# Performance work log

Hardware: AMD Instinct MI355X
Metric: run time of the kernel (lower is better)

The kernel has to match this reference:

```python
import jax, jax.numpy as jnp
import numpy as np
from functools import partial

D_MODEL = 768
N_LAYER = 2
VOCAB = 50264  # 50257 padded to multiple of 8
D_STATE = 16
D_INNER = 2 * D_MODEL
DT_RANK = 48
D_CONV = 4
EPS = 1e-5
ZOH_EPS = 1e-7
B, L = 2, 1024


def setup_inputs() -> dict:
    key = jax.random.key(0)
    ks = jax.random.split(key, 16)
    s = 0.02
    inp = {
        'input_ids': jax.random.randint(ks[0], (B, L), 0, VOCAB, dtype=jnp.int32),
        'embedding': jax.random.normal(ks[1], (VOCAB, D_MODEL), jnp.float32) * s,
        'in_w': jax.random.normal(ks[2], (N_LAYER, D_MODEL, 2 * D_INNER), jnp.float32) * s,
        'in_b': jnp.zeros((N_LAYER, 2 * D_INNER), jnp.float32),
        'conv_w': jax.random.normal(ks[3], (N_LAYER, D_INNER, D_CONV), jnp.float32) * s,
        'conv_b': jnp.zeros((N_LAYER, D_INNER), jnp.float32),
        'xproj_w': jax.random.normal(ks[4], (N_LAYER, D_INNER, DT_RANK + 2 * D_STATE), jnp.float32) * s,
        'dt_w': jax.random.normal(ks[5], (N_LAYER, DT_RANK, D_INNER), jnp.float32) * s,
        'dt_b': jnp.zeros((N_LAYER, D_INNER), jnp.float32),
        'A_log': jnp.broadcast_to(jnp.log(jnp.arange(1, D_STATE + 1, dtype=jnp.float32))[None, None, :], (N_LAYER, D_INNER, D_STATE)).copy(),
        'Dp': jnp.ones((N_LAYER, D_INNER), jnp.float32),
        'out_w': jax.random.normal(ks[6], (N_LAYER, D_INNER, D_MODEL), jnp.float32) * s,
        'out_b': jnp.zeros((N_LAYER, D_MODEL), jnp.float32),
        'norm_w': jnp.ones((N_LAYER, D_MODEL), jnp.float32),
        'normf_w': jnp.ones((D_MODEL,), jnp.float32),
    }
    return inp


def rmsnorm(x, w):
    return x * jax.lax.rsqrt(jnp.mean(x * x, axis=-1, keepdims=True) + EPS) * w


def mamba_block(x, in_w, in_b, conv_w, conv_b, xproj_w, dt_w, dt_b, A_log, Dp, out_w, out_b):
    # x: (b, l, d_model)
    xr = x @ in_w + in_b                       # (b, l, 2*d_inner)
    xi, res = jnp.split(xr, 2, axis=-1)        # each (b, l, d_inner)
    # causal depthwise conv1d (torch pads d_conv-1 both sides then truncates to l)
    xc = jnp.transpose(xi, (0, 2, 1))          # (b, d_inner, l)
    xc = jax.lax.conv_general_dilated(
        xc, conv_w[:, None, :], (1,), [(D_CONV - 1, 0)],
        dimension_numbers=('NCH', 'OIH', 'NCH'), feature_group_count=D_INNER)
    xc = xc + conv_b[None, :, None]
    u = jax.nn.silu(jnp.transpose(xc, (0, 2, 1)))  # (b, l, d_inner)
    res = jax.nn.silu(res)
    # generate time-varying SSM params
    dbc = u @ xproj_w                          # (b, l, dt_rank + 2n)
    dt, Bm, Cm = jnp.split(dbc, [DT_RANK, DT_RANK + D_STATE], axis=-1)
    delta = jax.nn.softplus(dt @ dt_w + dt_b)  # (b, l, d_inner)
    A = -jnp.exp(A_log)                        # (d_inner, n)
    # ZOH discretization
    dA = jnp.exp(jnp.einsum('bld,dn->bldn', delta, A))            # (b,l,d_in,n)
    zoh = (dA - 1.0) / (A + ZOH_EPS)                               # (b,l,d_in,n)
    dBu = zoh * Bm[:, :, None, :] * u[..., None]                   # (b,l,d_in,n)
    # selective scan over l
    def step(s, inputs):
        dA_t, dBu_t, C_t = inputs              # (b,d_in,n),(b,d_in,n),(b,n)
        s = dA_t * s + dBu_t
        y = jnp.einsum('bdn,bn->bd', s, C_t)
        return s, y
    s0 = jnp.zeros((u.shape[0], D_INNER, D_STATE), u.dtype)
    _, ys = jax.lax.scan(step, s0, (jnp.moveaxis(dA, 1, 0), jnp.moveaxis(dBu, 1, 0), jnp.moveaxis(Cm, 1, 0)))
    y = jnp.moveaxis(ys, 0, 1) + u * Dp        # (b, l, d_inner)
    y = y * res
    return y @ out_w + out_b


def forward(input_ids, embedding, in_w, in_b, conv_w, conv_b, xproj_w, dt_w, dt_b, A_log, Dp, out_w, out_b, norm_w, normf_w):
    x = embedding[input_ids]                   # (b, l, d_model)
    for i in range(N_LAYER):
        mixed = mamba_block(x, in_w[i], in_b[i], conv_w[i], conv_b[i], xproj_w[i],
                            dt_w[i], dt_b[i], A_log[i], Dp[i], out_w[i], out_b[i])
        x = rmsnorm(mixed + x, norm_w[i])      # ResidualBlock: norm(mixer(x)+x)
    x = rmsnorm(x, normf_w)
    return x @ embedding.T                     # tied lm_head, (b, l, vocab)


def reference(input_ids, embedding, in_w, in_b, conv_w, conv_b, xproj_w, dt_w, dt_b, A_log, Dp, out_w, out_b, norm_w, normf_w):
    return forward(input_ids, embedding, in_w, in_b, conv_w, conv_b, xproj_w,
                   dt_w, dt_b, A_log, Dp, out_w, out_b, norm_w, normf_w)
```

## Files before the change

kernel.cpp:

```cpp
#include <hip/hip_runtime.h>
#include <math.h>
#include <stdint.h>

#define BB 2
#define LL 1024
#define DM 768
#define NL 2
#define VV 50264
#define VPAD 50304
#define DS 16
#define DI 1536
#define DR 48
#define DC 4
#define MM (BB*LL)

#define CH 32
#define NC (LL/CH)

#define KS 8

#define TS 64
#define KT 16

typedef __attribute__((ext_vector_type(8))) short short8;
typedef __attribute__((ext_vector_type(4))) float f32x4;

#define AS3(p) ((__attribute__((address_space(3))) unsigned int*)(unsigned int)(uintptr_t)(p))
#define AS1(p) ((const __attribute__((address_space(1))) unsigned int*)(uintptr_t)(p))

__device__ __forceinline__ unsigned short f2bf(float v) {
    union { float f; unsigned u; } x; x.f = v;
    unsigned r = x.u + 0x7fffu + ((x.u >> 16) & 1u);
    return (unsigned short)(r >> 16);
}

__global__ __launch_bounds__(256) void embed_kernel(
    const int* __restrict__ ids, const float* __restrict__ emb,
    float* __restrict__ x, unsigned short* __restrict__ x16)
{
    int m = blockIdx.x;
    int v = ids[m];
    const float* src = emb + (size_t)v * DM;
    float* dst = x + (size_t)m * DM;
    unsigned short* dst16 = x16 + (size_t)m * DM;
    for (int i = threadIdx.x; i < DM; i += 256) {
        float f = src[i];
        dst[i] = f;
        dst16[i] = f2bf(f);
    }
}

__global__ __launch_bounds__(256) void emb_convert_kernel(
    const float* __restrict__ emb, unsigned short* __restrict__ out)
{
    size_t i8 = (size_t)blockIdx.x * 256 + threadIdx.x;
    size_t row = i8 / 96;
    size_t col8 = (i8 - row * 96) * 8;
    if (row >= VPAD) return;
    ushort4 o0, o1;
    if (row < VV) {
        const float* p = emb + row * DM + col8;
        float4 v0 = *(const float4*)p;
        float4 v1 = *(const float4*)(p + 4);
        o0.x = f2bf(v0.x); o0.y = f2bf(v0.y); o0.z = f2bf(v0.z); o0.w = f2bf(v0.w);
        o1.x = f2bf(v1.x); o1.y = f2bf(v1.y); o1.z = f2bf(v1.z); o1.w = f2bf(v1.w);
    } else {
        o0 = make_ushort4(0, 0, 0, 0);
        o1 = o0;
    }
    unsigned short* op = out + row * DM + col8;
    *(ushort4*)op = o0;
    *(ushort4*)(op + 4) = o1;
}

__global__ __launch_bounds__(256) void transpose_bf16_kernel(
    const float* __restrict__ in, unsigned short* __restrict__ out, int R, int C)
{
    __shared__ float t[32][33];
    int l = blockIdx.z;
    int r0 = blockIdx.y * 32, c0 = blockIdx.x * 32;
    int tx = threadIdx.x & 31, ty = threadIdx.x >> 5;
    const float* ip = in + (size_t)l * R * C;
    unsigned short* op = out + (size_t)l * C * R;
    #pragma unroll
    for (int j = 0; j < 32; j += 8)
        t[ty + j][tx] = ip[(size_t)(r0 + ty + j) * C + c0 + tx];
    __syncthreads();
    #pragma unroll
    for (int j = 0; j < 32; j += 8)
        op[(size_t)(c0 + ty + j) * R + r0 + tx] = f2bf(t[tx][ty + j]);
}

__global__ __launch_bounds__(256) void gemm_mfma_bt(
    const unsigned short* __restrict__ A, const unsigned short* __restrict__ B,
    const float* __restrict__ bias, const float* __restrict__ resid,
    float* __restrict__ C, int M, int N, int K, int MT, int NTILES)
{
    int T = MT * NTILES;
    int q = T >> 3, r = T & 7;
    int orig = blockIdx.x;
    int xcd = orig & 7, u = orig >> 3;
    int wg = (xcd < r ? xcd * (q + 1) : r * (q + 1) + (xcd - r) * q) + u;
    int mt = wg % MT, nt = wg / MT;

    __shared__ unsigned short As[3][128 * 32];
    __shared__ unsigned short Bs[3][128 * 32];
    int tid = threadIdx.x;
    int w = tid >> 6, lane = tid & 63;
    int m0 = mt * 128, n0 = nt * 128;

    int rA = lane >> 2;
    int kb = (lane & 3) * 8;
    const unsigned short* gA0 = A + (size_t)(m0 + w * 16 + rA) * K + kb;
    const unsigned short* gA1 = gA0 + (size_t)64 * K;
    const unsigned short* gB0 = B + (size_t)(n0 + w * 16 + rA) * K + kb;
    const unsigned short* gB1 = gB0 + (size_t)64 * K;

    int lr = lane & 15, lk = lane >> 4;
    int wr = (w >> 1) * 64, wc = (w & 1) * 64;

    f32x4 acc[4][4] = {};

#define STAGE(k0, buf) do { \
    __builtin_amdgcn_global_load_lds(AS1(gA0 + (k0)), AS3(&As[buf][(w * 16) * 32]), 16, 0, 0); \
    __builtin_amdgcn_global_load_lds(AS1(gA1 + (k0)), AS3(&As[buf][(64 + w * 16) * 32]), 16, 0, 0); \
    __builtin_amdgcn_global_load_lds(AS1(gB0 + (k0)), AS3(&Bs[buf][(w * 16) * 32]), 16, 0, 0); \
    __builtin_amdgcn_global_load_lds(AS1(gB1 + (k0)), AS3(&Bs[buf][(64 + w * 16) * 32]), 16, 0, 0); \
} while (0)

#define COMPUTE(buf) do { \
    short8 a[4], b[4]; \
    _Pragma("unroll") \
    for (int f = 0; f < 4; ++f) \
        a[f] = *(const short8*)&As[buf][(wr + f * 16 + lr) * 32 + lk * 8]; \
    _Pragma("unroll") \
    for (int f = 0; f < 4; ++f) \
        b[f] = *(const short8*)&Bs[buf][(wc + f * 16 + lr) * 32 + lk * 8]; \
    _Pragma("unroll") \
    for (int i = 0; i < 4; ++i) \
        _Pragma("unroll") \
        for (int j = 0; j < 4; ++j) \
            acc[i][j] = __builtin_amdgcn_mfma_f32_16x16x32_bf16(a[i], b[j], acc[i][j], 0, 0, 0); \
} while (0)

    int nsteps = K / 32;
    STAGE(0, 0);
    STAGE(32, 1);
    asm volatile("s_waitcnt vmcnt(4)" ::: "memory");
    __builtin_amdgcn_s_barrier();
    __builtin_amdgcn_sched_barrier(0);

    for (int t = 0; t < nsteps; ++t) {
        int cur = t % 3;
        if (t + 2 < nsteps)
            STAGE((t + 2) * 32, (t + 2) % 3);
        COMPUTE(cur);
        if (t + 1 < nsteps) {
            if (t + 2 < nsteps)
                asm volatile("s_waitcnt vmcnt(4)" ::: "memory");
            else
                asm volatile("s_waitcnt vmcnt(0)" ::: "memory");
            __builtin_amdgcn_s_barrier();
            __builtin_amdgcn_sched_barrier(0);
        }
    }

#undef STAGE
#undef COMPUTE

    #pragma unroll
    for (int i = 0; i < 4; ++i) {
        int row = m0 + wr + i * 16 + lk * 4;
        #pragma unroll
        for (int j = 0; j < 4; ++j) {
            int col = n0 + wc + j * 16 + lr;
            if (col < N) {
                float bv = bias ? bias[col] : 0.f;
                #pragma unroll
                for (int r2 = 0; r2 < 4; ++r2) {
                    float v = acc[i][j][r2] + bv;
                    if (resid) v += resid[(size_t)(row + r2) * N + col];
                    C[(size_t)(row + r2) * N + col] = v;
                }
            }
        }
    }
}

__global__ __launch_bounds__(512) void gemm_logits(
    const unsigned short* __restrict__ A, const unsigned short* __restrict__ B,
    float* __restrict__ C, int M, int N, int K, int MT, int NTILES)
{
    int T = MT * NTILES;
    int q = T >> 3, r = T & 7;
    int orig = blockIdx.x;
    int xcd = orig & 7, u = orig >> 3;
    int wg = (xcd < r ? xcd * (q + 1) : r * (q + 1) + (xcd - r) * q) + u;
    int mt = wg % MT, nt = wg / MT;

    __shared__ unsigned short As[3][256 * 32];
    __shared__ unsigned short Bs[3][128 * 32];
    int tid = threadIdx.x;
    int w = tid >> 6, lane = tid & 63;
    int wm = w >> 1, wn = w & 1;
    int m0 = mt * 256, n0 = nt * 128;

    int srow = tid >> 2;
    int schunk = (tid & 3) ^ ((srow & 3) ^ ((srow >> 2) & 3));
    const unsigned short* gA0 = A + (size_t)(m0 + srow) * K + schunk * 8;
    const unsigned short* gA1 = gA0 + (size_t)128 * K;
    const unsigned short* gB0 = B + (size_t)(n0 + srow) * K + schunk * 8;

    int lr = lane & 15, lk = lane >> 4;
    int rc = (lk ^ ((lr & 3) ^ ((lr >> 2) & 3))) * 8;

    f32x4 acc[4][4] = {};

#define STAGE_A(k0, buf) do { \
    __builtin_amdgcn_global_load_lds(AS1(gA0 + (k0)), AS3(&As[buf][(w * 16) * 32]), 16, 0, 0); \
    __builtin_amdgcn_global_load_lds(AS1(gA1 + (k0)), AS3(&As[buf][(128 + w * 16) * 32]), 16, 0, 0); \
} while (0)
#define STAGE_B(k0, buf) do { \
    __builtin_amdgcn_global_load_lds(AS1(gB0 + (k0)), AS3(&Bs[buf][(w * 16) * 32]), 16, 0, 0); \
} while (0)

    int nsteps = K / 32;

    STAGE_A(0, 0); STAGE_B(0, 0);
    STAGE_A(32, 1); STAGE_B(32, 1);
    asm volatile("s_waitcnt vmcnt(3)" ::: "memory");
    __builtin_amdgcn_s_barrier();
    __builtin_amdgcn_sched_barrier(0);

    for (int t = 0; t < nsteps; ++t) {
        int s = t % 3;
        int sn = (t + 2) % 3;
        bool stage2 = (t + 2) < nsteps;
        short8 av[2], bv[4];

        #pragma unroll
        for (int f = 0; f < 2; ++f)
            av[f] = *(const short8*)&As[s][(wm * 64 + f * 16 + lr) * 32 + rc];
        #pragma unroll
        for (int f = 0; f < 4; ++f)
            bv[f] = *(const short8*)&Bs[s][(wn * 64 + f * 16 + lr) * 32 + rc];
        if (stage2) STAGE_A((t + 2) * 32, sn);
        __builtin_amdgcn_s_barrier();
        asm volatile("s_waitcnt lgkmcnt(0)" ::: "memory");
        __builtin_amdgcn_sched_barrier(0);
        __builtin_amdgcn_s_setprio(1);
        #pragma unroll
        for (int i = 0; i < 2; ++i)
            #pragma unroll
            for (int j = 0; j < 4; ++j)
                acc[i][j] = __builtin_amdgcn_mfma_f32_16x16x32_bf16(av[i], bv[j], acc[i][j], 0, 0, 0);
        __builtin_amdgcn_s_setprio(0);
        __builtin_amdgcn_s_barrier();

        #pragma unroll
        for (int f = 0; f < 2; ++f)
            av[f] = *(const short8*)&As[s][(wm * 64 + (2 + f) * 16 + lr) * 32 + rc];
        if (stage2) STAGE_B((t + 2) * 32, sn);
        __builtin_amdgcn_s_barrier();
        asm volatile("s_waitcnt lgkmcnt(0)" ::: "memory");
        __builtin_amdgcn_sched_barrier(0);
        __builtin_amdgcn_s_setprio(1);
        #pragma unroll
        for (int i = 0; i < 2; ++i)
            #pragma unroll
            for (int j = 0; j < 4; ++j)
                acc[2 + i][j] = __builtin_amdgcn_mfma_f32_16x16x32_bf16(av[i], bv[j], acc[2 + i][j], 0, 0, 0);
        __builtin_amdgcn_s_setprio(0);

        if (t + 1 < nsteps) {
            if (stage2)
                asm volatile("s_waitcnt vmcnt(3)" ::: "memory");
            else
                asm volatile("s_waitcnt vmcnt(0)" ::: "memory");
            __builtin_amdgcn_s_barrier();
            __builtin_amdgcn_sched_barrier(0);
        }
    }

#undef STAGE_A
#undef STAGE_B

    #pragma unroll
    for (int i = 0; i < 4; ++i) {
        int row = m0 + wm * 64 + i * 16 + lk * 4;
        #pragma unroll
        for (int j = 0; j < 4; ++j) {
            int col = n0 + wn * 64 + j * 16 + lr;
            if (col < N) {
                #pragma unroll
                for (int r2 = 0; r2 < 4; ++r2)
                    C[(size_t)(row + r2) * N + col] = acc[i][j][r2];
            }
        }
    }
}

template<int ACT>
__global__ __launch_bounds__(256) void gemm_tiled(
    const float* __restrict__ A, const float* __restrict__ Bm,
    const float* __restrict__ bias, float* __restrict__ C,
    int M, int N, int K, int lda)
{
    __shared__ float As[KT][TS + 4];
    __shared__ float Bs[KT][TS + 4];
    int tid = threadIdx.x;
    int tx = tid & 15, ty = tid >> 4;
    int m0 = blockIdx.y * TS;
    int n0 = blockIdx.x * TS;
    float acc[4][4] = {};

    for (int k0 = 0; k0 < K; k0 += KT) {
        {
            int i = tid >> 2;
            int k4 = (tid & 3) * 4;
            int m = m0 + i;
            float4 v = make_float4(0.f, 0.f, 0.f, 0.f);
            if (m < M) v = *(const float4*)(A + (size_t)m * lda + k0 + k4);
            As[k4 + 0][i] = v.x; As[k4 + 1][i] = v.y;
            As[k4 + 2][i] = v.z; As[k4 + 3][i] = v.w;
        }
        {
            int k = tid >> 4;
            int j4 = (tid & 15) * 4;
            int n = n0 + j4;
            float4 v = make_float4(0.f, 0.f, 0.f, 0.f);
            const float* p = Bm + (size_t)(k0 + k) * N + n;
            if (n + 3 < N) {
                v = *(const float4*)p;
            } else {
                float t0 = (n + 0 < N) ? p[0] : 0.f;
                float t1 = (n + 1 < N) ? p[1] : 0.f;
                float t2 = (n + 2 < N) ? p[2] : 0.f;
                float t3 = (n + 3 < N) ? p[3] : 0.f;
                v = make_float4(t0, t1, t2, t3);
            }
            Bs[k][j4 + 0] = v.x; Bs[k][j4 + 1] = v.y;
            Bs[k][j4 + 2] = v.z; Bs[k][j4 + 3] = v.w;
        }
        __syncthreads();
        #pragma unroll
        for (int k = 0; k < KT; ++k) {
            float a[4], b[4];
            #pragma unroll
            for (int q2 = 0; q2 < 4; ++q2) a[q2] = As[k][ty * 4 + q2];
            #pragma unroll
            for (int q2 = 0; q2 < 4; ++q2) b[q2] = Bs[k][tx * 4 + q2];
            #pragma unroll
            for (int i = 0; i < 4; ++i)
                #pragma unroll
                for (int j = 0; j < 4; ++j)
                    acc[i][j] = fmaf(a[i], b[j], acc[i][j]);
        }
        __syncthreads();
    }

    #pragma unroll
    for (int i = 0; i < 4; ++i) {
        int m = m0 + ty * 4 + i;
        if (m >= M) continue;
        #pragma unroll
        for (int j = 0; j < 4; ++j) {
            int n = n0 + tx * 4 + j;
            if (n >= N) continue;
            float v = acc[i][j];
            if (bias)  v += bias[n];
            if (ACT == 1) v = fmaxf(v, 0.f) + log1pf(expf(-fabsf(v)));
            C[(size_t)m * N + n] = v;
        }
    }
}

__global__ __launch_bounds__(256) void xproj_part_kernel(
    const float* __restrict__ A, const float* __restrict__ Bm, float* __restrict__ part)
{
    __shared__ float As[KT][TS + 4];
    __shared__ float Bs[KT][TS + 4];
    int tid = threadIdx.x;
    int tx = tid & 15, ty = tid >> 4;
    int m0 = blockIdx.y * TS;
    int n0 = blockIdx.x * TS;
    int kbeg = blockIdx.z * (DI / KS);
    const int N = 80;
    float acc[4][4] = {};

    for (int k0 = kbeg; k0 < kbeg + DI / KS; k0 += KT) {
        {
            int i = tid >> 2;
            int k4 = (tid & 3) * 4;
            float4 v = *(const float4*)(A + (size_t)(m0 + i) * DI + k0 + k4);
            As[k4 + 0][i] = v.x; As[k4 + 1][i] = v.y;
            As[k4 + 2][i] = v.z; As[k4 + 3][i] = v.w;
        }
        {
            int k = tid >> 4;
            int j4 = (tid & 15) * 4;
            int n = n0 + j4;
            const float* p = Bm + (size_t)(k0 + k) * N + n;
            float4 v;
            if (n + 3 < N) {
                v = *(const float4*)p;
            } else {
                v.x = (n + 0 < N) ? p[0] : 0.f;
                v.y = (n + 1 < N) ? p[1] : 0.f;
                v.z = (n + 2 < N) ? p[2] : 0.f;
                v.w = (n + 3 < N) ? p[3] : 0.f;
            }
            Bs[k][j4 + 0] = v.x; Bs[k][j4 + 1] = v.y;
            Bs[k][j4 + 2] = v.z; Bs[k][j4 + 3] = v.w;
        }
        __syncthreads();
        #pragma unroll
        for (int k = 0; k < KT; ++k) {
            float a[4], b[4];
            #pragma unroll
            for (int q2 = 0; q2 < 4; ++q2) a[q2] = As[k][ty * 4 + q2];
            #pragma unroll
            for (int q2 = 0; q2 < 4; ++q2) b[q2] = Bs[k][tx * 4 + q2];
            #pragma unroll
            for (int i = 0; i < 4; ++i)
                #pragma unroll
                for (int j = 0; j < 4; ++j)
                    acc[i][j] = fmaf(a[i], b[j], acc[i][j]);
        }
        __syncthreads();
    }

    float* op = part + (size_t)blockIdx.z * MM * 80;
    #pragma unroll
    for (int i = 0; i < 4; ++i) {
        int m = m0 + ty * 4 + i;
        #pragma unroll
        for (int j = 0; j < 4; ++j) {
            int n = n0 + tx * 4 + j;
            if (n < 80) op[(size_t)m * 80 + n] = acc[i][j];
        }
    }
}

__global__ __launch_bounds__(256) void xproj_reduce_kernel(
    const float* __restrict__ part, float* __restrict__ dbc)
{
    int i = blockIdx.x * 256 + threadIdx.x;
    if (i >= MM * 80) return;
    float s = 0.f;
    #pragma unroll
    for (int z = 0; z < KS; ++z) s += part[(size_t)z * MM * 80 + i];
    dbc[i] = s;
}

__global__ __launch_bounds__(256) void conv_silu_kernel(
    const float* __restrict__ xr, const float* __restrict__ cw,
    const float* __restrict__ cb, float* __restrict__ u)
{
    int d = blockIdx.x * 256 + threadIdx.x;
    int l = blockIdx.y;
    int b = blockIdx.z;
    float acc = cb[d];
    #pragma unroll
    for (int j = 0; j < DC; ++j) {
        int lp = l - (DC - 1) + j;
        if (lp >= 0)
            acc = fmaf(xr[((size_t)(b * LL + lp)) * (2 * DI) + d], cw[d * DC + j], acc);
    }
    float s = acc / (1.f + expf(-acc));
    u[((size_t)(b * LL + l)) * DI + d] = s;
}

__global__ __launch_bounds__(256) void scan_reduce_kernel(
    const float* __restrict__ delta, const float* __restrict__ u,
    const float* __restrict__ dbc, const float* __restrict__ A_log,
    float* __restrict__ P, float* __restrict__ Q)
{
    int d = blockIdx.x * 256 + threadIdx.x;
    int c = blockIdx.y;
    int b = blockIdx.z;

    float Av[DS], invA[DS];
    {
        const float4* ap = (const float4*)(A_log + (size_t)d * DS);
        #pragma unroll
        for (int n4 = 0; n4 < 4; ++n4) {
            float4 a = ap[n4];
            Av[n4 * 4 + 0] = -expf(a.x); Av[n4 * 4 + 1] = -expf(a.y);
            Av[n4 * 4 + 2] = -expf(a.z); Av[n4 * 4 + 3] = -expf(a.w);
        }
        #pragma unroll
        for (int n = 0; n < DS; ++n) invA[n] = 1.f / (Av[n] + 1e-7f);
    }

    float p[DS], s[DS];
    #pragma unroll
    for (int n = 0; n < DS; ++n) { p[n] = 1.f; s[n] = 0.f; }

    const float* dp = delta + ((size_t)b * LL + c * CH) * DI + d;
    const float* up = u     + ((size_t)b * LL + c * CH) * DI + d;
    const float* bb = dbc   + ((size_t)b * LL + c * CH) * 80 + DR;

    for (int l = 0; l < CH; ++l) {
        float dlt = dp[(size_t)l * DI];
        float uv  = up[(size_t)l * DI];
        float Bv[DS];
        {
            const float4* bp4 = (const float4*)(bb + (size_t)l * 80);
            #pragma unroll
            for (int n4 = 0; n4 < 4; ++n4) {
                float4 v = bp4[n4];
                Bv[n4 * 4 + 0] = v.x; Bv[n4 * 4 + 1] = v.y;
                Bv[n4 * 4 + 2] = v.z; Bv[n4 * 4 + 3] = v.w;
            }
        }
        #pragma unroll
        for (int n = 0; n < DS; ++n) {
            float dA = expf(dlt * Av[n]);
            float dBu = (dA - 1.f) * invA[n] * Bv[n] * uv;
            p[n] *= dA;
            s[n] = fmaf(dA, s[n], dBu);
        }
    }

    float* Pp = P + (((size_t)b * NC + c) * DI + d) * DS;
    float* Qp = Q + (((size_t)b * NC + c) * DI + d) * DS;
    #pragma unroll
    for (int n4 = 0; n4 < 4; ++n4) {
        ((float4*)Pp)[n4] = make_float4(p[n4 * 4 + 0], p[n4 * 4 + 1], p[n4 * 4 + 2], p[n4 * 4 + 3]);
        ((float4*)Qp)[n4] = make_float4(s[n4 * 4 + 0], s[n4 * 4 + 1], s[n4 * 4 + 2], s[n4 * 4 + 3]);
    }
}

__global__ __launch_bounds__(256) void scan_apply_kernel(
    const float* __restrict__ delta, const float* __restrict__ u,
    const float* __restrict__ dbc, const float* __restrict__ xr,
    const float* __restrict__ A_log, const float* __restrict__ Dp,
    const float* __restrict__ P, const float* __restrict__ Q,
    unsigned short* __restrict__ y16)
{
    int d = blockIdx.x * 256 + threadIdx.x;
    int c = blockIdx.y;
    int b = blockIdx.z;

    float Av[DS], invA[DS];
    {
        const float4* ap = (const float4*)(A_log + (size_t)d * DS);
        #pragma unroll
        for (int n4 = 0; n4 < 4; ++n4) {
            float4 a = ap[n4];
            Av[n4 * 4 + 0] = -expf(a.x); Av[n4 * 4 + 1] = -expf(a.y);
            Av[n4 * 4 + 2] = -expf(a.z); Av[n4 * 4 + 3] = -expf(a.w);
        }
        #pragma unroll
        for (int n = 0; n < DS; ++n) invA[n] = 1.f / (Av[n] + 1e-7f);
    }
    float Dv = Dp[d];

    float s[DS];
    #pragma unroll
    for (int n = 0; n < DS; ++n) s[n] = 0.f;
    for (int cc = 0; cc < c; ++cc) {
        const float* Pp = P + (((size_t)b * NC + cc) * DI + d) * DS;
        const float* Qp = Q + (((size_t)b * NC + cc) * DI + d) * DS;
        float pv[DS], qv[DS];
        #pragma unroll
        for (int n4 = 0; n4 < 4; ++n4) {
            float4 pw = ((const float4*)Pp)[n4];
            float4 qw = ((const float4*)Qp)[n4];
            pv[n4 * 4 + 0] = pw.x; pv[n4 * 4 + 1] = pw.y; pv[n4 * 4 + 2] = pw.z; pv[n4 * 4 + 3] = pw.w;
            qv[n4 * 4 + 0] = qw.x; qv[n4 * 4 + 1] = qw.y; qv[n4 * 4 + 2] = qw.z; qv[n4 * 4 + 3] = qw.w;
        }
        #pragma unroll
        for (int n = 0; n < DS; ++n) s[n] = fmaf(pv[n], s[n], qv[n]);
    }

    const float* dp = delta + ((size_t)b * LL + c * CH) * DI + d;
    const float* up = u     + ((size_t)b * LL + c * CH) * DI + d;
    const float* xp = xr    + ((size_t)b * LL + c * CH) * (2 * DI) + DI + d;
    const float* bb = dbc   + ((size_t)b * LL + c * CH) * 80 + DR;
    unsigned short* yp = y16 + ((size_t)b * LL + c * CH) * DI + d;

    for (int l = 0; l < CH; ++l) {
        float dlt = dp[(size_t)l * DI];
        float uv  = up[(size_t)l * DI];
        float rv  = xp[(size_t)l * (2 * DI)];
        float Bv[DS], Cv[DS];
        {
            const float4* bp4 = (const float4*)(bb + (size_t)l * 80);
            #pragma unroll
            for (int n4 = 0; n4 < 4; ++n4) {
                float4 v = bp4[n4];
                Bv[n4 * 4 + 0] = v.x; Bv[n4 * 4 + 1] = v.y;
                Bv[n4 * 4 + 2] = v.z; Bv[n4 * 4 + 3] = v.w;
            }
            #pragma unroll
            for (int n4 = 0; n4 < 4; ++n4) {
                float4 v = bp4[4 + n4];
                Cv[n4 * 4 + 0] = v.x; Cv[n4 * 4 + 1] = v.y;
                Cv[n4 * 4 + 2] = v.z; Cv[n4 * 4 + 3] = v.w;
            }
        }
        float pv = 0.f;
        #pragma unroll
        for (int n = 0; n < DS; ++n) {
            float dA = expf(dlt * Av[n]);
            float dBu = (dA - 1.f) * invA[n] * Bv[n] * uv;
            s[n] = fmaf(dA, s[n], dBu);
            pv = fmaf(s[n], Cv[n], pv);
        }
        float res = rv / (1.f + expf(-rv));
        yp[(size_t)l * DI] = f2bf((pv + uv * Dv) * res);
    }
}

__global__ __launch_bounds__(256) void rmsnorm_kernel(
    const float* __restrict__ in, const float* __restrict__ w,
    float* __restrict__ outf, unsigned short* __restrict__ outb)
{
    int m = blockIdx.x;
    const float* row = in + (size_t)m * DM;
    float ss = 0.f;
    for (int i = threadIdx.x; i < DM; i += 256) { float v = row[i]; ss = fmaf(v, v, ss); }
    #pragma unroll
    for (int off = 32; off > 0; off >>= 1) ss += __shfl_down(ss, off);
    __shared__ float sred[4];
    __shared__ float sscale;
    int wid = threadIdx.x >> 6;
    if ((threadIdx.x & 63) == 0) sred[wid] = ss;
    __syncthreads();
    if (threadIdx.x == 0) {
        float tot = sred[0] + sred[1] + sred[2] + sred[3];
        sscale = 1.f / sqrtf(tot / (float)DM + 1e-5f);
    }
    __syncthreads();
    float sc = sscale;
    for (int i = threadIdx.x; i < DM; i += 256) {
        float v = row[i] * sc * w[i];
        if (outf) outf[(size_t)m * DM + i] = v;
        if (outb) outb[(size_t)m * DM + i] = f2bf(v);
    }
}

extern "C" void kernel_launch(void* const* d_in, const int* in_sizes, int n_in,
                              void* d_out, int out_size, void* d_ws, size_t ws_size,
                              hipStream_t stream)
{
    const int*   ids      = (const int*)  d_in[0];
    const float* emb      = (const float*)d_in[1];
    const float* in_w     = (const float*)d_in[2];
    const float* in_b     = (const float*)d_in[3];
    const float* conv_w   = (const float*)d_in[4];
    const float* conv_b   = (const float*)d_in[5];
    const float* xproj_w  = (const float*)d_in[6];
    const float* dt_w     = (const float*)d_in[7];
    const float* dt_b     = (const float*)d_in[8];
    const float* A_log    = (const float*)d_in[9];
    const float* Dp       = (const float*)d_in[10];
    const float* out_w    = (const float*)d_in[11];
    const float* out_b    = (const float*)d_in[12];
    const float* norm_w   = (const float*)d_in[13];
    const float* normf_w  = (const float*)d_in[14];
    float* out = (float*)d_out;

    char* wsp = (char*)d_ws;
    auto alloc = [&](size_t bytes) {
        char* p = wsp;
        wsp += (bytes + 255) & ~(size_t)255;
        return p;
    };
    float* x     = (float*)alloc((size_t)MM * DM * 4);
    float* xr    = (float*)alloc((size_t)MM * 2 * DI * 4);
    float* u     = (float*)alloc((size_t)MM * DI * 4);
    float* dbc   = (float*)alloc((size_t)MM * 80 * 4);
    float* part  = (float*)alloc((size_t)KS * MM * 80 * 4);
    float* delta = (float*)alloc((size_t)MM * DI * 4);
    float* tmp   = (float*)alloc((size_t)MM * DM * 4);
    float* Pbuf  = (float*)alloc((size_t)BB * NC * DI * DS * 4);
    float* Qbuf  = (float*)alloc((size_t)BB * NC * DI * DS * 4);
    unsigned short* x16     = (unsigned short*)alloc((size_t)MM * DM * 2);
    unsigned short* y16     = (unsigned short*)alloc((size_t)MM * DI * 2);
    unsigned short* emb16   = (unsigned short*)alloc((size_t)VPAD * DM * 2);
    unsigned short* in_wT   = (unsigned short*)alloc((size_t)NL * 2 * DI * DM * 2);
    unsigned short* out_wT  = (unsigned short*)alloc((size_t)NL * DM * DI * 2);

    emb_convert_kernel<<<((size_t)VPAD * (DM / 8) + 255) / 256, 256, 0, stream>>>(emb, emb16);
    transpose_bf16_kernel<<<dim3(2 * DI / 32, DM / 32, NL), 256, 0, stream>>>(
        in_w, in_wT, DM, 2 * DI);
    transpose_bf16_kernel<<<dim3(DM / 32, DI / 32, NL), 256, 0, stream>>>(
        out_w, out_wT, DI, DM);

    embed_kernel<<<MM, 256, 0, stream>>>(ids, emb, x, x16);

    for (int layer = 0; layer < NL; ++layer) {
        const float* lb_in  = in_b    + (size_t)layer * 2 * DI;
        const float* lcw    = conv_w  + (size_t)layer * DI * DC;
        const float* lcb    = conv_b  + (size_t)layer * DI;
        const float* lxw    = xproj_w + (size_t)layer * DI * (DR + 2 * DS);
        const float* ldtw   = dt_w    + (size_t)layer * DR * DI;
        const float* ldtb   = dt_b    + (size_t)layer * DI;
        const float* lAlog  = A_log   + (size_t)layer * DI * DS;
        const float* lDp    = Dp      + (size_t)layer * DI;
        const float* lob    = out_b   + (size_t)layer * DM;
        const float* lnw    = norm_w  + (size_t)layer * DM;
        const unsigned short* lw_inT = in_wT  + (size_t)layer * 2 * DI * DM;
        const unsigned short* lw_outT= out_wT + (size_t)layer * DM * DI;

        gemm_mfma_bt<<<16 * 24, 256, 0, stream>>>(
            x16, lw_inT, lb_in, nullptr, xr, MM, 2 * DI, DM, 16, 24);

        conv_silu_kernel<<<dim3(DI / 256, LL, BB), 256, 0, stream>>>(xr, lcw, lcb, u);

        xproj_part_kernel<<<dim3(2, MM / TS, KS), 256, 0, stream>>>(u, lxw, part);
        xproj_reduce_kernel<<<(MM * 80 + 255) / 256, 256, 0, stream>>>(part, dbc);

        gemm_tiled<1><<<dim3(DI / TS, MM / TS), 256, 0, stream>>>(
            dbc, ldtw, ldtb, delta, MM, DI, DR, DR + 2 * DS);

        scan_reduce_kernel<<<dim3(DI / 256, NC, BB), 256, 0, stream>>>(
            delta, u, dbc, lAlog, Pbuf, Qbuf);
        scan_apply_kernel<<<dim3(DI / 256, NC, BB), 256, 0, stream>>>(
            delta, u, dbc, xr, lAlog, lDp, Pbuf, Qbuf, y16);

        gemm_mfma_bt<<<16 * 6, 256, 0, stream>>>(
            y16, lw_outT, lob, x, tmp, MM, DM, DI, 16, 6);

        rmsnorm_kernel<<<MM, 256, 0, stream>>>(tmp, lnw, x, x16);
    }

    rmsnorm_kernel<<<MM, 256, 0, stream>>>(x, normf_w, nullptr, x16);

    gemm_logits<<<8 * (VPAD / 128), 512, 0, stream>>>(
        x16, emb16, out, MM, VV, DM, 8, VPAD / 128);
}
```

Measured before the change: 801.9 us.

## Split-K out-projection with fused norm, chunk-prefix scan combine, and blocked conv

The out-projection GEMM becomes a split-K kernel over two K halves, raising the block count from 96 to 192. A fused rmsnorm kernel then sums both partials with the bias and residual. The quadratic per-chunk prefix loop in scan_apply is replaced by a separate combine kernel that computes each chunk's initial state once, so apply blocks no longer reread all earlier chunk summaries. The conv+silu kernel now processes 16 timesteps per thread with a sliding register window, cutting redundant loads. In exchange the change adds two extra partial buffers, an extra state buffer and one more launch.

```diff
diff --git a/kernel.cpp b/kernel.cpp
--- a/kernel.cpp
+++ b/kernel.cpp
@@ -16,6 +16,7 @@
 
 #define CH 32
 #define NC (LL/CH)
+#define CONVL 16
 
 #define KS 8
 
@@ -183,6 +184,99 @@
                     C[(size_t)(row + r2) * N + col] = v;
                 }
             }
+        }
+    }
+}
+
+__global__ __launch_bounds__(256) void gemm_out_part(
+    const unsigned short* __restrict__ A, const unsigned short* __restrict__ B,
+    float* __restrict__ part)
+{
+    const int T = 16 * 6 * 2;
+    int q = T >> 3;
+    int orig = blockIdx.x;
+    int xcd = orig & 7, u = orig >> 3;
+    int wg = xcd * q + u;
+    int mt = wg % 16;
+    int rest = wg / 16;
+    int nt = rest % 6, z = rest / 6;
+
+    __shared__ unsigned short As[3][128 * 32];
+    __shared__ unsigned short Bs[3][128 * 32];
+    int tid = threadIdx.x;
+    int w = tid >> 6, lane = tid & 63;
+    int m0 = mt * 128, n0 = nt * 128;
+    int kh = z * 768;
+
+    int rA = lane >> 2;
+    int kb = (lane & 3) * 8;
+    const unsigned short* gA0 = A + (size_t)(m0 + w * 16 + rA) * DI + kh + kb;
+    const unsigned short* gA1 = gA0 + (size_t)64 * DI;
+    const unsigned short* gB0 = B + (size_t)(n0 + w * 16 + rA) * DI + kh + kb;
+    const unsigned short* gB1 = gB0 + (size_t)64 * DI;
+
+    int lr = lane & 15, lk = lane >> 4;
+    int wr = (w >> 1) * 64, wc = (w & 1) * 64;
+
+    f32x4 acc[4][4] = {};
+
+#define STAGE(k0, buf) do { \
+    __builtin_amdgcn_global_load_lds(AS1(gA0 + (k0)), AS3(&As[buf][(w * 16) * 32]), 16, 0, 0); \
+    __builtin_amdgcn_global_load_lds(AS1(gA1 + (k0)), AS3(&As[buf][(64 + w * 16) * 32]), 16, 0, 0); \
+    __builtin_amdgcn_global_load_lds(AS1(gB0 + (k0)), AS3(&Bs[buf][(w * 16) * 32]), 16, 0, 0); \
+    __builtin_amdgcn_global_load_lds(AS1(gB1 + (k0)), AS3(&Bs[buf][(64 + w * 16) * 32]), 16, 0, 0); \
+} while (0)
+
+#define COMPUTE(buf) do { \
+    short8 a[4], b[4]; \
+    _Pragma("unroll") \
+    for (int f = 0; f < 4; ++f) \
+        a[f] = *(const short8*)&As[buf][(wr + f * 16 + lr) * 32 + lk * 8]; \
+    _Pragma("unroll") \
+    for (int f = 0; f < 4; ++f) \
+        b[f] = *(const short8*)&Bs[buf][(wc + f * 16 + lr) * 32 + lk * 8]; \
+    _Pragma("unroll") \
+    for (int i = 0; i < 4; ++i) \
+        _Pragma("unroll") \
+        for (int j = 0; j < 4; ++j) \
+            acc[i][j] = __builtin_amdgcn_mfma_f32_16x16x32_bf16(a[i], b[j], acc[i][j], 0, 0, 0); \
+} while (0)
+
+    const int nsteps = 768 / 32;
+    STAGE(0, 0);
+    STAGE(32, 1);
+    asm volatile("s_waitcnt vmcnt(4)" ::: "memory");
+    __builtin_amdgcn_s_barrier();
+    __builtin_amdgcn_sched_barrier(0);
+
+    for (int t = 0; t < nsteps; ++t) {
+        int cur = t % 3;
+        if (t + 2 < nsteps)
+            STAGE((t + 2) * 32, (t + 2) % 3);
+        COMPUTE(cur);
+        if (t + 1 < nsteps) {
+            if (t + 2 < nsteps)
+                asm volatile("s_waitcnt vmcnt(4)" ::: "memory");
+            else
+                asm volatile("s_waitcnt vmcnt(0)" ::: "memory");
+            __builtin_amdgcn_s_barrier();
+            __builtin_amdgcn_sched_barrier(0);
+        }
+    }
+
+#undef STAGE
+#undef COMPUTE
+
+    float* op = part + (size_t)z * MM * DM;
+    #pragma unroll
+    for (int i = 0; i < 4; ++i) {
+        int row = m0 + wr + i * 16 + lk * 4;
+        #pragma unroll
+        for (int j = 0; j < 4; ++j) {
+            int col = n0 + wc + j * 16 + lr;
+            #pragma unroll
+            for (int r2 = 0; r2 < 4; ++r2)
+                op[(size_t)(row + r2) * DM + col] = acc[i][j][r2];
         }
     }
 }
@@ -458,17 +552,28 @@
     const float* __restrict__ cb, float* __restrict__ u)
 {
     int d = blockIdx.x * 256 + threadIdx.x;
-    int l = blockIdx.y;
+    int l0 = blockIdx.y * CONVL;
     int b = blockIdx.z;
-    float acc = cb[d];
-    #pragma unroll
-    for (int j = 0; j < DC; ++j) {
-        int lp = l - (DC - 1) + j;
-        if (lp >= 0)
-            acc = fmaf(xr[((size_t)(b * LL + lp)) * (2 * DI) + d], cw[d * DC + j], acc);
-    }
-    float s = acc / (1.f + expf(-acc));
-    u[((size_t)(b * LL + l)) * DI + d] = s;
+    const float4 wv = *(const float4*)(cw + (size_t)d * DC);
+    float bias = cb[d];
+    const float* xp = xr + ((size_t)(b * LL + l0)) * (2 * DI) + d;
+    float* up = u + ((size_t)(b * LL + l0)) * DI + d;
+    const ptrdiff_t RS = 2 * DI;
+    float xm3 = (l0 >= 3) ? xp[-3 * RS] : 0.f;
+    float xm2 = (l0 >= 2) ? xp[-2 * RS] : 0.f;
+    float xm1 = (l0 >= 1) ? xp[-1 * RS] : 0.f;
+    #pragma unroll
+    for (int l = 0; l < CONVL; ++l) {
+        float xc = xp[(ptrdiff_t)l * RS];
+        float acc = bias;
+        acc = fmaf(wv.x, xm3, acc);
+        acc = fmaf(wv.y, xm2, acc);
+        acc = fmaf(wv.z, xm1, acc);
+        acc = fmaf(wv.w, xc, acc);
+        float s = acc / (1.f + expf(-acc));
+        up[(size_t)l * DI] = s;
+        xm3 = xm2; xm2 = xm1; xm1 = xc;
+    }
 }
 
 __global__ __launch_bounds__(256) void scan_reduce_kernel(
@@ -532,12 +637,25 @@
     }
 }
 
+__global__ __launch_bounds__(256) void scan_combine_kernel(
+    const float* __restrict__ P, const float* __restrict__ Q, float* __restrict__ Sinit)
+{
+    int t = blockIdx.x * 256 + threadIdx.x;
+    int b = t / (DI * DS);
+    int dn = t - b * (DI * DS);
+    float s = 0.f;
+    for (int c = 0; c < NC; ++c) {
+        size_t idx = ((size_t)b * NC + c) * (DI * DS) + dn;
+        Sinit[idx] = s;
+        s = fmaf(P[idx], s, Q[idx]);
+    }
+}
+
 __global__ __launch_bounds__(256) void scan_apply_kernel(
     const float* __restrict__ delta, const float* __restrict__ u,
     const float* __restrict__ dbc, const float* __restrict__ xr,
     const float* __restrict__ A_log, const float* __restrict__ Dp,
-    const float* __restrict__ P, const float* __restrict__ Q,
-    unsigned short* __restrict__ y16)
+    const float* __restrict__ Sinit, unsigned short* __restrict__ y16)
 {
     int d = blockIdx.x * 256 + threadIdx.x;
     int c = blockIdx.y;
@@ -558,21 +676,14 @@
     float Dv = Dp[d];
 
     float s[DS];
-    #pragma unroll
-    for (int n = 0; n < DS; ++n) s[n] = 0.f;
-    for (int cc = 0; cc < c; ++cc) {
-        const float* Pp = P + (((size_t)b * NC + cc) * DI + d) * DS;
-        const float* Qp = Q + (((size_t)b * NC + cc) * DI + d) * DS;
-        float pv[DS], qv[DS];
+    {
+        const float4* Sp = (const float4*)(Sinit + (((size_t)b * NC + c) * DI + d) * DS);
         #pragma unroll
         for (int n4 = 0; n4 < 4; ++n4) {
-            float4 pw = ((const float4*)Pp)[n4];
-            float4 qw = ((const float4*)Qp)[n4];
-            pv[n4 * 4 + 0] = pw.x; pv[n4 * 4 + 1] = pw.y; pv[n4 * 4 + 2] = pw.z; pv[n4 * 4 + 3] = pw.w;
-            qv[n4 * 4 + 0] = qw.x; qv[n4 * 4 + 1] = qw.y; qv[n4 * 4 + 2] = qw.z; qv[n4 * 4 + 3] = qw.w;
-        }
-        #pragma unroll
-        for (int n = 0; n < DS; ++n) s[n] = fmaf(pv[n], s[n], qv[n]);
+            float4 sw = Sp[n4];
+            s[n4 * 4 + 0] = sw.x; s[n4 * 4 + 1] = sw.y;
+            s[n4 * 4 + 2] = sw.z; s[n4 * 4 + 3] = sw.w;
+        }
     }
 
     const float* dp = delta + ((size_t)b * LL + c * CH) * DI + d;
@@ -640,6 +751,44 @@
         if (outf) outf[(size_t)m * DM + i] = v;
         if (outb) outb[(size_t)m * DM + i] = f2bf(v);
     }
+}
+
+__global__ __launch_bounds__(256) void rmsnorm_fuse_kernel(
+    const float* __restrict__ p0, const float* __restrict__ p1,
+    const float* __restrict__ ob, const float* __restrict__ w,
+    float* __restrict__ x, unsigned short* __restrict__ x16)
+{
+    int m = blockIdx.x;
+    int tid = threadIdx.x;
+    float v0, v1, v2;
+    float ss = 0.f;
+    {
+        size_t base = (size_t)m * DM;
+        v0 = p0[base + tid] + p1[base + tid] + x[base + tid] + ob[tid];
+        v1 = p0[base + tid + 256] + p1[base + tid + 256] + x[base + tid + 256] + ob[tid + 256];
+        v2 = p0[base + tid + 512] + p1[base + tid + 512] + x[base + tid + 512] + ob[tid + 512];
+        ss = fmaf(v0, v0, fmaf(v1, v1, v2 * v2));
+    }
+    #pragma unroll
+    for (int off = 32; off > 0; off >>= 1) ss += __shfl_down(ss, off);
+    __shared__ float sred[4];
+    __shared__ float sscale;
+    int wid = tid >> 6;
+    if ((tid & 63) == 0) sred[wid] = ss;
+    __syncthreads();
+    if (tid == 0) {
+        float tot = sred[0] + sred[1] + sred[2] + sred[3];
+        sscale = 1.f / sqrtf(tot / (float)DM + 1e-5f);
+    }
+    __syncthreads();
+    float sc = sscale;
+    size_t base = (size_t)m * DM;
+    float o0 = v0 * sc * w[tid];
+    float o1 = v1 * sc * w[tid + 256];
+    float o2 = v2 * sc * w[tid + 512];
+    x[base + tid] = o0;         x16[base + tid] = f2bf(o0);
+    x[base + tid + 256] = o1;   x16[base + tid + 256] = f2bf(o1);
+    x[base + tid + 512] = o2;   x16[base + tid + 512] = f2bf(o2);
 }
 
 extern "C" void kernel_launch(void* const* d_in, const int* in_sizes, int n_in,
@@ -675,9 +824,10 @@
     float* dbc   = (float*)alloc((size_t)MM * 80 * 4);
     float* part  = (float*)alloc((size_t)KS * MM * 80 * 4);
     float* delta = (float*)alloc((size_t)MM * DI * 4);
-    float* tmp   = (float*)alloc((size_t)MM * DM * 4);
+    float* oprt  = (float*)alloc((size_t)2 * MM * DM * 4);
     float* Pbuf  = (float*)alloc((size_t)BB * NC * DI * DS * 4);
     float* Qbuf  = (float*)alloc((size_t)BB * NC * DI * DS * 4);
+    float* Sbuf  = (float*)alloc((size_t)BB * NC * DI * DS * 4);
     unsigned short* x16     = (unsigned short*)alloc((size_t)MM * DM * 2);
     unsigned short* y16     = (unsigned short*)alloc((size_t)MM * DI * 2);
     unsigned short* emb16   = (unsigned short*)alloc((size_t)VPAD * DM * 2);
@@ -709,7 +859,7 @@
         gemm_mfma_bt<<<16 * 24, 256, 0, stream>>>(
             x16, lw_inT, lb_in, nullptr, xr, MM, 2 * DI, DM, 16, 24);
 
-        conv_silu_kernel<<<dim3(DI / 256, LL, BB), 256, 0, stream>>>(xr, lcw, lcb, u);
+        conv_silu_kernel<<<dim3(DI / 256, LL / CONVL, BB), 256, 0, stream>>>(xr, lcw, lcb, u);
 
         xproj_part_kernel<<<dim3(2, MM / TS, KS), 256, 0, stream>>>(u, lxw, part);
         xproj_reduce_kernel<<<(MM * 80 + 255) / 256, 256, 0, stream>>>(part, dbc);
@@ -719,13 +869,14 @@
 
         scan_reduce_kernel<<<dim3(DI / 256, NC, BB), 256, 0, stream>>>(
             delta, u, dbc, lAlog, Pbuf, Qbuf);
+        scan_combine_kernel<<<(BB * DI * DS) / 256, 256, 0, stream>>>(Pbuf, Qbuf, Sbuf);
         scan_apply_kernel<<<dim3(DI / 256, NC, BB), 256, 0, stream>>>(
-            delta, u, dbc, xr, lAlog, lDp, Pbuf, Qbuf, y16);
-
-        gemm_mfma_bt<<<16 * 6, 256, 0, stream>>>(
-            y16, lw_outT, lob, x, tmp, MM, DM, DI, 16, 6);
-
-        rmsnorm_kernel<<<MM, 256, 0, stream>>>(tmp, lnw, x, x16);
+            delta, u, dbc, xr, lAlog, lDp, Sbuf, y16);
+
+        gemm_out_part<<<192, 256, 0, stream>>>(y16, lw_outT, oprt);
+
+        rmsnorm_fuse_kernel<<<MM, 256, 0, stream>>>(
+            oprt, oprt + (size_t)MM * DM, lob, lnw, x, x16);
     }
 
     rmsnorm_kernel<<<MM, 256, 0, stream>>>(x, normf_w, nullptr, x16);
```

After: 739.5 us (median of 2 runs). -7.8%, faster.
